# Kernel optimization log

Measured on AMD Instinct MI355X. Metric: run time of the kernel, lower is better.

The kernel has to match this reference:

```python
import jax, jax.numpy as jnp
import numpy as np

DIM = 512
HEADS = 8
DIM_HEAD = 64
B, N = 4, 2048
EPS = 1e-5


def setup_inputs() -> dict:
    key = jax.random.key(0)
    ks = jax.random.split(key, 6)
    s = 0.02
    x = jax.random.normal(ks[0], (B, N, DIM), dtype=jnp.float32)
    Wq = jax.random.normal(ks[1], (DIM, HEADS * DIM_HEAD), dtype=jnp.float32) * s
    Wkv = jax.random.normal(ks[2], (DIM, 2 * HEADS * DIM_HEAD), dtype=jnp.float32) * s
    Wo = jax.random.normal(ks[3], (HEADS * DIM_HEAD, DIM), dtype=jnp.float32) * s
    bo = jnp.zeros((DIM,), dtype=jnp.float32)
    # gating layer: torch init is weight=0, bias=1; randomize weight slightly for a nontrivial path
    Wg = jax.random.normal(ks[4], (DIM, HEADS * DIM_HEAD), dtype=jnp.float32) * s
    bg = jnp.ones((HEADS * DIM_HEAD,), dtype=jnp.float32)
    gamma = jnp.ones((DIM,), dtype=jnp.float32)
    beta = jnp.zeros((DIM,), dtype=jnp.float32)
    return {"x": x, "Wq": Wq, "Wkv": Wkv, "Wo": Wo, "bo": bo,
            "Wg": Wg, "bg": bg, "gamma": gamma, "beta": beta}


def reference(x, Wq, Wkv, Wo, bo, Wg, bg, gamma, beta):
    h, d = HEADS, DIM_HEAD
    scale = d ** -0.5
    b, n, _ = x.shape

    q = x @ Wq                                   # [b, n, h*d]
    kv = x @ Wkv                                 # [b, n, 2*h*d]
    k, v = jnp.split(kv, 2, axis=-1)

    def split_heads(t):
        return t.reshape(b, n, h, d).transpose(0, 2, 1, 3)  # [b, h, n, d]

    q = split_heads(q) * scale
    k = split_heads(k)
    v = split_heads(v)

    dots = jnp.einsum('bhid,bhjd->bhij', q, k)   # [b, h, n, n]
    attn = jax.nn.softmax(dots, axis=-1)
    out = jnp.einsum('bhij,bhjd->bhid', attn, v)  # [b, h, n, d]
    out = out.transpose(0, 2, 1, 3).reshape(b, n, h * d)

    gates = x @ Wg + bg                           # [b, n, h*d]
    out = out * jax.nn.sigmoid(gates)
    out = out @ Wo + bo                           # [b, n, dim]
    out = x + out

    # LayerNorm over last dim, eps=1e-5 (torch default)
    mu = jnp.mean(out, axis=-1, keepdims=True)
    var = jnp.var(out, axis=-1, keepdims=True)
    out = (out - mu) * jax.lax.rsqrt(var + EPS) * gamma + beta
    return out
```

## Files before the change

### kernel.cpp

```cpp
#include <hip/hip_runtime.h>
#include <hip/hip_bf16.h>
#include <stdint.h>
#include <stddef.h>

#define SEQ   2048
#define NBATCH 4
#define NHEAD  8
#define DMODEL 512

typedef __attribute__((ext_vector_type(8))) short bf16x8;
typedef __attribute__((ext_vector_type(4))) float f32x4;
typedef __attribute__((ext_vector_type(16))) float f32x16;

#define MFMA16(a, b, c) __builtin_amdgcn_mfma_f32_16x16x32_bf16(a, b, c, 0, 0, 0)
#define MFMA32(a, b, c) __builtin_amdgcn_mfma_f32_32x32x16_bf16(a, b, c, 0, 0, 0)

#define QSCALE 0.18033688011112042f

__device__ __forceinline__ float bf2f(ushort u) {
  union { uint32_t i; float f; } v; v.i = ((uint32_t)u) << 16; return v.f;
}
__device__ __forceinline__ ushort f2bf(float f) {
  union { float f; uint32_t i; } v; v.f = f;
  uint32_t u = v.i;
  return (ushort)((u + 0x7fffu + ((u >> 16) & 1u)) >> 16);
}
__device__ __forceinline__ uint32_t cvtpk(float lo, float hi) {
  uint32_t d;
  asm("v_cvt_pk_bf16_f32 %0, %1, %2" : "=v"(d) : "v"(lo), "v"(hi));
  return d;
}

#if __has_builtin(__builtin_amdgcn_global_load_lds)
__device__ __forceinline__ void gload16(const void* g, void* l) {
  __builtin_amdgcn_global_load_lds(
      (const __attribute__((address_space(1))) void*)g,
      (__attribute__((address_space(3))) void*)l, 16, 0, 0);
}
#define GLOAD_DIRECT 1
#else
#define GLOAD_DIRECT 0
#endif

__global__ __launch_bounds__(256) void prep_k(const float* __restrict__ x,
                                              const float* __restrict__ Wq,
                                              const float* __restrict__ Wkv,
                                              const float* __restrict__ Wg,
                                              const float* __restrict__ Wo,
                                              ushort* __restrict__ xb,
                                              ushort* __restrict__ WT,
                                              ushort* __restrict__ WoT) {
  __shared__ ushort tile[32][33];
  int t = threadIdx.x;
  if (blockIdx.x < 2048) {
    int i = blockIdx.x * 256 + t;
    const float4* p = (const float4*)(x + (size_t)i * 8);
    float4 a = p[0], b = p[1];
    union { int4 v; ushort u[8]; } o;
    o.u[0] = f2bf(a.x); o.u[1] = f2bf(a.y); o.u[2] = f2bf(a.z); o.u[3] = f2bf(a.w);
    o.u[4] = f2bf(b.x); o.u[5] = f2bf(b.y); o.u[6] = f2bf(b.z); o.u[7] = f2bf(b.w);
    *(int4*)(xb + (size_t)i * 8) = o.v;
    return;
  }
  int bidx = blockIdx.x - 2048;
  int bx = bidx % 80, by = bidx / 80;
  const float* W;
  ushort* dst;
  int N, nt;
  if (bx < 16)       { W = Wq;  dst = WT;              N = 512;  nt = bx; }
  else if (bx < 48)  { W = Wkv; dst = WT + 512 * 512;  N = 1024; nt = bx - 16; }
  else if (bx < 64)  { W = Wg;  dst = WT + 1536 * 512; N = 512;  nt = bx - 48; }
  else               { W = Wo;  dst = WoT;             N = 512;  nt = bx - 64; }
  int n0 = nt * 32, k0 = by * 32;
  int r = t >> 3, c = (t & 7) * 4;
#pragma unroll
  for (int j = 0; j < 4; j++)
    tile[r][c + j] = f2bf(W[(size_t)(k0 + r) * N + n0 + c + j]);
  __syncthreads();
#pragma unroll
  for (int j = 0; j < 4; j++)
    dst[(size_t)(n0 + r) * 512 + k0 + c + j] = tile[c + j][r];
}

__global__ __launch_bounds__(256, 2) void gemm128_k(const ushort* __restrict__ A,
                                                    const ushort* __restrict__ Bt,
                                                    ushort* __restrict__ qb,
                                                    ushort* __restrict__ kb,
                                                    ushort* __restrict__ vT,
                                                    ushort* __restrict__ gsb,
                                                    const float* __restrict__ bias) {
  __shared__ __align__(16) ushort Sh[4 * 128 * 64];
#define ASB(p) (Sh + (p) * (128 * 64))
#define BSB(p) (Sh + 2 * (128 * 64) + (p) * (128 * 64))
  int t = threadIdx.x;
  int nb = gridDim.x * gridDim.y;
  int bid = blockIdx.y * gridDim.x + blockIdx.x;
  int swz = (bid & 7) * (nb >> 3) + (bid >> 3);
  int row0 = (swz / gridDim.x) * 128, col0 = (swz % gridDim.x) * 128;

  int w = t >> 6, l = t & 63, l31 = l & 31, hi = l >> 5;
  int wm = w >> 1, wn = w & 1;
  f32x16 acc[2][2] = {};

  int srow = t >> 3;
  int ssl = (t & 7) ^ (srow & 7);
  const ushort* Ag = A + (size_t)(row0 + srow) * 512 + ssl * 8;
  const ushort* Bg = Bt + (size_t)(col0 + srow) * 512 + ssl * 8;
  int wslot = __builtin_amdgcn_readfirstlane((t >> 6) << 6);

#if GLOAD_DIRECT
#define STG(p, kt)                                                              \
  do {                                                                          \
    gload16(Ag + (size_t)(kt) * 64 + 0 * 32 * 512, ASB(p) + (wslot +   0) * 8); \
    gload16(Ag + (size_t)(kt) * 64 + 1 * 32 * 512, ASB(p) + (wslot + 256) * 8); \
    gload16(Ag + (size_t)(kt) * 64 + 2 * 32 * 512, ASB(p) + (wslot + 512) * 8); \
    gload16(Ag + (size_t)(kt) * 64 + 3 * 32 * 512, ASB(p) + (wslot + 768) * 8); \
    gload16(Bg + (size_t)(kt) * 64 + 0 * 32 * 512, BSB(p) + (wslot +   0) * 8); \
    gload16(Bg + (size_t)(kt) * 64 + 1 * 32 * 512, BSB(p) + (wslot + 256) * 8); \
    gload16(Bg + (size_t)(kt) * 64 + 2 * 32 * 512, BSB(p) + (wslot + 512) * 8); \
    gload16(Bg + (size_t)(kt) * 64 + 3 * 32 * 512, BSB(p) + (wslot + 768) * 8); \
  } while (0)
#else
#define STG(p, kt)                                                                  \
  do {                                                                              \
    *(int4*)(ASB(p) + (t +   0) * 8) = *(const int4*)(Ag + (size_t)(kt) * 64);      \
    *(int4*)(ASB(p) + (t + 256) * 8) =                                              \
        *(const int4*)(Ag + (size_t)(kt) * 64 + 1 * 32 * 512);                      \
    *(int4*)(ASB(p) + (t + 512) * 8) =                                              \
        *(const int4*)(Ag + (size_t)(kt) * 64 + 2 * 32 * 512);                      \
    *(int4*)(ASB(p) + (t + 768) * 8) =                                              \
        *(const int4*)(Ag + (size_t)(kt) * 64 + 3 * 32 * 512);                      \
    *(int4*)(BSB(p) + (t +   0) * 8) = *(const int4*)(Bg + (size_t)(kt) * 64);      \
    *(int4*)(BSB(p) + (t + 256) * 8) =                                              \
        *(const int4*)(Bg + (size_t)(kt) * 64 + 1 * 32 * 512);                      \
    *(int4*)(BSB(p) + (t + 512) * 8) =                                              \
        *(const int4*)(Bg + (size_t)(kt) * 64 + 2 * 32 * 512);                      \
    *(int4*)(BSB(p) + (t + 768) * 8) =                                              \
        *(const int4*)(Bg + (size_t)(kt) * 64 + 3 * 32 * 512);                      \
  } while (0)
#endif

#define FRAG(Mb, r, s) \
  (*(const bf16x8*)(Mb + ((r) * 64) + ((((s) ^ ((r) & 7))) << 3)))

  STG(0, 0);
  __syncthreads();

  for (int kt = 0; kt < 8; kt++) {
    int p = kt & 1;
    if (kt < 7) STG(p ^ 1, kt + 1);

    bf16x8 bfrag[2][4];
#pragma unroll
    for (int cb = 0; cb < 2; cb++)
#pragma unroll
      for (int kk = 0; kk < 4; kk++)
        bfrag[cb][kk] = FRAG(BSB(p), wn * 64 + cb * 32 + l31, kk * 2 + hi);

    __builtin_amdgcn_s_setprio(1);
#pragma unroll
    for (int rb = 0; rb < 2; rb++) {
      bf16x8 af[4];
#pragma unroll
      for (int kk = 0; kk < 4; kk++)
        af[kk] = FRAG(ASB(p), wm * 64 + rb * 32 + l31, kk * 2 + hi);
#pragma unroll
      for (int kk = 0; kk < 4; kk++) {
        acc[rb][0] = MFMA32(af[kk], bfrag[0][kk], acc[rb][0]);
        acc[rb][1] = MFMA32(af[kk], bfrag[1][kk], acc[rb][1]);
      }
    }
    __builtin_amdgcn_s_setprio(0);

    if (kt < 7) __syncthreads();
  }
#undef STG
#undef FRAG

  if (col0 >= 1024 && col0 < 1536) {
    __syncthreads();
    ushort* lt = Sh;
#pragma unroll
    for (int rb = 0; rb < 2; rb++)
#pragma unroll
      for (int cb = 0; cb < 2; cb++)
#pragma unroll
        for (int e = 0; e < 16; e++) {
          int rr = (e & 3) + 8 * (e >> 2) + 4 * hi;
          int rowL = wm * 64 + rb * 32 + rr;
          int colL = wn * 64 + cb * 32 + l31;
          lt[colL * 136 + rowL] = f2bf(acc[rb][cb][e]);
        }
    __syncthreads();
    int b_ = row0 >> 11;
    int nb0 = row0 & 2047;
#pragma unroll
    for (int r = 0; r < 8; r++) {
      int lin = r * 256 + t;
      int dcol = lin >> 4, n8 = lin & 15;
      int vcol = (col0 - 1024) + dcol;
      int hh = vcol >> 6, dd = vcol & 63;
      bf16x8 v = *(const bf16x8*)(lt + dcol * 136 + n8 * 8);
      *(bf16x8*)(vT + (((size_t)(b_ * 8 + hh) * 64) + dd) * 2048 + nb0 + n8 * 8) = v;
    }
  } else {
#pragma unroll
    for (int rb = 0; rb < 2; rb++) {
#pragma unroll
      for (int cb = 0; cb < 2; cb++) {
#pragma unroll
        for (int e = 0; e < 16; e++) {
          int rr = (e & 3) + 8 * (e >> 2) + 4 * hi;
          int row = row0 + wm * 64 + rb * 32 + rr;
          int col = col0 + wn * 64 + cb * 32 + l31;
          float v = acc[rb][cb][e];
          if (col0 < 512) {
            qb[(size_t)row * 512 + col] = f2bf(v * QSCALE);
          } else if (col0 < 1024) {
            kb[(size_t)row * 512 + (col - 512)] = f2bf(v);
          } else {
            v += bias[col - 1536];
            v = 1.f / (1.f + __expf(-v));
            gsb[(size_t)row * 512 + (col - 1536)] = f2bf(v);
          }
        }
      }
    }
  }
#undef ASB
#undef BSB
}

__global__ __launch_bounds__(256, 2) void gemm_o_k(const ushort* __restrict__ A,
                                                   const ushort* __restrict__ Bt,
                                                   float* __restrict__ yout,
                                                   const float* __restrict__ bias,
                                                   const float* __restrict__ res) {
  __shared__ __align__(16) ushort As[2][128 * 64];
  __shared__ __align__(16) ushort Bs[2][64 * 64];
  int t = threadIdx.x;
  int nb = gridDim.x * gridDim.y;
  int bid = blockIdx.y * gridDim.x + blockIdx.x;
  int swz = (bid & 7) * (nb >> 3) + (bid >> 3);
  int row0 = (swz / gridDim.x) * 128, col0 = (swz % gridDim.x) * 64;

  int w = t >> 6, l = t & 63, l31 = l & 31, hi = l >> 5;
  int wm = w >> 1, wn = w & 1;
  f32x16 acc[2] = {};

  int srow = t >> 3;
  int ssl = (t & 7) ^ (srow & 7);
  const ushort* Ag = A + (size_t)(row0 + srow) * 512 + ssl * 8;
  const ushort* Bg = Bt + (size_t)(col0 + srow) * 512 + ssl * 8;
  int wslot = __builtin_amdgcn_readfirstlane((t >> 6) << 6);

#if GLOAD_DIRECT
#define STG(p, kt)                                                                \
  do {                                                                            \
    gload16(Ag + (size_t)(kt) * 64 + 0 * 32 * 512, &As[p][(wslot +   0) * 8]);    \
    gload16(Ag + (size_t)(kt) * 64 + 1 * 32 * 512, &As[p][(wslot + 256) * 8]);    \
    gload16(Ag + (size_t)(kt) * 64 + 2 * 32 * 512, &As[p][(wslot + 512) * 8]);    \
    gload16(Ag + (size_t)(kt) * 64 + 3 * 32 * 512, &As[p][(wslot + 768) * 8]);    \
    gload16(Bg + (size_t)(kt) * 64 + 0 * 32 * 512, &Bs[p][(wslot +   0) * 8]);    \
    gload16(Bg + (size_t)(kt) * 64 + 1 * 32 * 512, &Bs[p][(wslot + 256) * 8]);    \
  } while (0)
#else
#define STG(p, kt)                                                                  \
  do {                                                                              \
    *(int4*)(&As[p][(t +   0) * 8]) = *(const int4*)(Ag + (size_t)(kt) * 64);       \
    *(int4*)(&As[p][(t + 256) * 8]) =                                               \
        *(const int4*)(Ag + (size_t)(kt) * 64 + 1 * 32 * 512);                      \
    *(int4*)(&As[p][(t + 512) * 8]) =                                               \
        *(const int4*)(Ag + (size_t)(kt) * 64 + 2 * 32 * 512);                      \
    *(int4*)(&As[p][(t + 768) * 8]) =                                               \
        *(const int4*)(Ag + (size_t)(kt) * 64 + 3 * 32 * 512);                      \
    *(int4*)(&Bs[p][(t +   0) * 8]) = *(const int4*)(Bg + (size_t)(kt) * 64);       \
    *(int4*)(&Bs[p][(t + 256) * 8]) =                                               \
        *(const int4*)(Bg + (size_t)(kt) * 64 + 1 * 32 * 512);                      \
  } while (0)
#endif

#define FRAG(Mb, r, s) \
  (*(const bf16x8*)(&(Mb)[((r) * 64) + ((((s) ^ ((r) & 7))) << 3)]))

  STG(0, 0);
  __syncthreads();

  for (int kt = 0; kt < 8; kt++) {
    int p = kt & 1;
    if (kt < 7) STG(p ^ 1, kt + 1);

    bf16x8 bfrag[4];
#pragma unroll
    for (int kk = 0; kk < 4; kk++)
      bfrag[kk] = FRAG(Bs[p], wn * 32 + l31, kk * 2 + hi);

    __builtin_amdgcn_s_setprio(1);
#pragma unroll
    for (int rb = 0; rb < 2; rb++) {
      bf16x8 af[4];
#pragma unroll
      for (int kk = 0; kk < 4; kk++)
        af[kk] = FRAG(As[p], wm * 64 + rb * 32 + l31, kk * 2 + hi);
#pragma unroll
      for (int kk = 0; kk < 4; kk++)
        acc[rb] = MFMA32(af[kk], bfrag[kk], acc[rb]);
    }
    __builtin_amdgcn_s_setprio(0);

    if (kt < 7) __syncthreads();
  }
#undef STG
#undef FRAG

#pragma unroll
  for (int rb = 0; rb < 2; rb++) {
#pragma unroll
    for (int e = 0; e < 16; e++) {
      int rr = (e & 3) + 8 * (e >> 2) + 4 * hi;
      int row = row0 + wm * 64 + rb * 32 + rr;
      int col = col0 + wn * 32 + l31;
      float v = acc[rb][e] + bias[col] + res[(size_t)row * 512 + col];
      yout[(size_t)row * 512 + col] = v;
    }
  }
}

__global__ __launch_bounds__(512) void attn_k(const ushort* __restrict__ q,
                                              const ushort* __restrict__ kbuf,
                                              const ushort* __restrict__ vT,
                                              const ushort* __restrict__ gs,
                                              ushort* __restrict__ gated) {
  __shared__ __align__(16) ushort Kl[2][2][64][72];
  __shared__ __align__(16) ushort Vl[2][2][64][72];
  int t = threadIdx.x;
  int bid = blockIdx.x;
  int swz = (bid & 7) * 32 + (bid >> 3);
  int qt = swz & 7, bh = swz >> 3;
  int b = bh >> 3, h = bh & 7;
  int q0 = qt * 256;
  int w = t >> 6, l = t & 63;
  int l31 = l & 31, hi = l >> 5;
  size_t base_n = (size_t)b * SEQ;

  const ushort* qp = q + (base_n + q0 + w * 32 + l31) * 512 + h * 64 + hi * 8;
  bf16x8 qf[4];
#pragma unroll
  for (int kd = 0; kd < 4; kd++)
    qf[kd] = *(const bf16x8*)(qp + kd * 16);

  bf16x8 vones;
#pragma unroll
  for (int j = 0; j < 8; j++) vones[j] = (short)0x3F80;

  f32x16 acco0 = {}, acco1 = {}, acco2 = {};

  int srow = t >> 3, c8 = (t & 7) * 8;
  const ushort* kg = kbuf + (base_n + srow) * 512 + h * 64 + c8;
  const ushort* vg = vT + ((size_t)bh * 64 + srow) * 2048 + c8;

#define QK_PHASE(KB, S0, S1)                                                   \
  do {                                                                         \
    _Pragma("unroll")                                                          \
    for (int kd = 0; kd < 4; kd++) {                                           \
      bf16x8 k0 = *(const bf16x8*)((KB) + l31 * 144 + kd * 32 + hi * 16);      \
      bf16x8 k1 = *(const bf16x8*)((KB) + (32 + l31) * 144 + kd * 32 + hi * 16);\
      S0 = MFMA32(k0, qf[kd], S0);                                             \
      S1 = MFMA32(k1, qf[kd], S1);                                             \
    }                                                                          \
  } while (0)

#define SM_PHASE(S0, S1, PK)                                                   \
  do {                                                                         \
    _Pragma("unroll")                                                          \
    for (int sg = 0; sg < 4; sg++) {                                           \
      _Pragma("unroll")                                                        \
      for (int u = 0; u < 2; u++) {                                            \
        float a = __builtin_amdgcn_exp2f(S0[(sg << 2) | (u << 1)]);            \
        float c = __builtin_amdgcn_exp2f(S0[(sg << 2) | (u << 1) | 1]);        \
        PK[sg * 2 + u] = cvtpk(a, c);                                          \
      }                                                                        \
    }                                                                          \
    _Pragma("unroll")                                                          \
    for (int sg = 0; sg < 4; sg++) {                                           \
      _Pragma("unroll")                                                        \
      for (int u = 0; u < 2; u++) {                                            \
        float a = __builtin_amdgcn_exp2f(S1[(sg << 2) | (u << 1)]);            \
        float c = __builtin_amdgcn_exp2f(S1[(sg << 2) | (u << 1) | 1]);        \
        PK[8 + sg * 2 + u] = cvtpk(a, c);                                      \
      }                                                                        \
    }                                                                          \
  } while (0)

#define PV_PHASE(VB, PK)                                                       \
  do {                                                                         \
    _Pragma("unroll")                                                          \
    for (int jk = 0; jk < 4; jk++) {                                           \
      uint32_t x0 = PK[(2 * jk) * 2 + 0], y0 = PK[(2 * jk + 1) * 2 + 0];       \
      uint32_t x1 = PK[(2 * jk) * 2 + 1], y1 = PK[(2 * jk + 1) * 2 + 1];       \
      asm("v_permlane32_swap_b32 %0, %1" : "+v"(x0), "+v"(y0));                \
      asm("v_permlane32_swap_b32 %0, %1" : "+v"(x1), "+v"(y1));                \
      union { bf16x8 v; uint32_t u[4]; } pa;                                   \
      pa.u[0] = x0; pa.u[1] = x1; pa.u[2] = y0; pa.u[3] = y1;                  \
      bf16x8 v0 = *(const bf16x8*)((VB) + l31 * 144 + jk * 32 + hi * 16);      \
      bf16x8 v1 = *(const bf16x8*)((VB) + (32 + l31) * 144 + jk * 32 + hi * 16);\
      acco0 = MFMA32(pa.v, v0, acco0);                                         \
      acco1 = MFMA32(pa.v, v1, acco1);                                         \
      acco2 = MFMA32(pa.v, vones, acco2);                                      \
    }                                                                          \
  } while (0)

#define STAGE_LDS(pp)                                                          \
  do {                                                                         \
    *(int4*)((char*)Kl[pp][0] + srow * 144 + c8 * 2) = kA;                     \
    *(int4*)((char*)Kl[pp][1] + srow * 144 + c8 * 2) = kB;                     \
    *(int4*)((char*)Vl[pp][0] + srow * 144 + c8 * 2) = vA;                     \
    *(int4*)((char*)Vl[pp][1] + srow * 144 + c8 * 2) = vB;                     \
  } while (0)

#define LOADT(n)                                                               \
  do {                                                                         \
    kA = *(const int4*)(kg + (size_t)(n) * 128 * 512);                         \
    kB = *(const int4*)(kg + ((size_t)(n) * 128 + 64) * 512);                  \
    vA = *(const int4*)(vg + (n) * 128);                                       \
    vB = *(const int4*)(vg + (n) * 128 + 64);                                  \
  } while (0)

  int4 kA, kB, vA, vB;
  LOADT(0);
  STAGE_LDS(0);
  LOADT(1);
  __syncthreads();

  int p = 0;
  const int NT = SEQ / 128;
  for (int jt = 0; jt < NT; jt++) {
    f32x16 s0 = {}, s1 = {};
    __builtin_amdgcn_s_setprio(1);
    QK_PHASE((const char*)Kl[p][0], s0, s1);
    __builtin_amdgcn_s_setprio(0);
    if (jt < NT - 1) STAGE_LDS(p ^ 1);
    {
      uint32_t pk[16];
      SM_PHASE(s0, s1, pk);
      __builtin_amdgcn_s_setprio(1);
      PV_PHASE((const char*)Vl[p][0], pk);
      __builtin_amdgcn_s_setprio(0);
    }
    s0 = (f32x16){}; s1 = (f32x16){};
    __builtin_amdgcn_s_setprio(1);
    QK_PHASE((const char*)Kl[p][1], s0, s1);
    __builtin_amdgcn_s_setprio(0);
    {
      uint32_t pk[16];
      SM_PHASE(s0, s1, pk);
      __builtin_amdgcn_s_setprio(1);
      PV_PHASE((const char*)Vl[p][1], pk);
      __builtin_amdgcn_s_setprio(0);
    }

    if (jt < NT - 1) {
      __syncthreads();
      if (jt < NT - 2) LOADT(jt + 2);
      p ^= 1;
    }
  }
#undef QK_PHASE
#undef SM_PHASE
#undef PV_PHASE
#undef STAGE_LDS
#undef LOADT

#pragma unroll
  for (int e = 0; e < 16; e++) {
    int qr = (e & 3) + 8 * (e >> 2) + 4 * hi;
    size_t row = base_n + q0 + w * 32 + qr;
    int col = h * 64 + l31;
    float rcp = 1.f / acco2[e];
    float v0 = acco0[e] * rcp * bf2f(gs[row * 512 + col]);
    float v1 = acco1[e] * rcp * bf2f(gs[row * 512 + col + 32]);
    gated[row * 512 + col] = f2bf(v0);
    gated[row * 512 + col + 32] = f2bf(v1);
  }
}

__global__ __launch_bounds__(256) void ln_k(const float* __restrict__ y,
                                            const float* __restrict__ gamma,
                                            const float* __restrict__ beta,
                                            float* __restrict__ out) {
  int w = threadIdx.x >> 6, l = threadIdx.x & 63;
  size_t row = (size_t)blockIdx.x * 4 + w;
  const float4* yp = (const float4*)(y + row * 512);
  float4 a = yp[l * 2], b = yp[l * 2 + 1];
  float f[8] = {a.x, a.y, a.z, a.w, b.x, b.y, b.z, b.w};
  float sm = 0.f, sq = 0.f;
#pragma unroll
  for (int j = 0; j < 8; j++) { sm += f[j]; sq += f[j] * f[j]; }
#pragma unroll
  for (int off = 1; off < 64; off <<= 1) {
    sm += __shfl_xor(sm, off);
    sq += __shfl_xor(sq, off);
  }
  float mean = sm * (1.f / 512.f);
  float var = sq * (1.f / 512.f) - mean * mean;
  float rs = rsqrtf(var + 1e-5f);
  float4 g0 = ((const float4*)gamma)[l * 2], g1 = ((const float4*)gamma)[l * 2 + 1];
  float4 b0 = ((const float4*)beta)[l * 2],  b1 = ((const float4*)beta)[l * 2 + 1];
  float4 o0, o1;
  o0.x = (f[0] - mean) * rs * g0.x + b0.x;
  o0.y = (f[1] - mean) * rs * g0.y + b0.y;
  o0.z = (f[2] - mean) * rs * g0.z + b0.z;
  o0.w = (f[3] - mean) * rs * g0.w + b0.w;
  o1.x = (f[4] - mean) * rs * g1.x + b1.x;
  o1.y = (f[5] - mean) * rs * g1.y + b1.y;
  o1.z = (f[6] - mean) * rs * g1.z + b1.z;
  o1.w = (f[7] - mean) * rs * g1.w + b1.w;
  float4* op = (float4*)(out + row * 512);
  op[l * 2] = o0;
  op[l * 2 + 1] = o1;
}

extern "C" void kernel_launch(void* const* d_in, const int* in_sizes, int n_in,
                              void* d_out, int out_size, void* d_ws, size_t ws_size,
                              hipStream_t stream) {
  (void)in_sizes; (void)n_in; (void)out_size; (void)ws_size;
  const float* x     = (const float*)d_in[0];
  const float* Wq    = (const float*)d_in[1];
  const float* Wkv   = (const float*)d_in[2];
  const float* Wo    = (const float*)d_in[3];
  const float* bo    = (const float*)d_in[4];
  const float* Wg    = (const float*)d_in[5];
  const float* bg    = (const float*)d_in[6];
  const float* gamma = (const float*)d_in[7];
  const float* beta  = (const float*)d_in[8];

  char* ws = (char*)d_ws;
  ushort* xb    = (ushort*)(ws);
  ushort* qbuf  = (ushort*)(ws + (8u  << 20));
  ushort* kbuf  = (ushort*)(ws + (16u << 20));
  ushort* vT    = (ushort*)(ws + (32u << 20));
  ushort* gsb   = (ushort*)(ws + (40u << 20));
  ushort* gated = (ushort*)(ws + (48u << 20));
  float*  y     = (float*)(ws + (56u << 20));
  ushort* WT    = (ushort*)(ws + (72u << 20));
  ushort* WoT   = (ushort*)(ws + (74u << 20));

  prep_k<<<2048 + 1280, 256, 0, stream>>>(x, Wq, Wkv, Wg, Wo, xb, WT, WoT);

  gemm128_k<<<dim3(16, 64), 256, 0, stream>>>(xb, WT, qbuf, kbuf, vT, gsb, bg);

  attn_k<<<256, 512, 0, stream>>>(qbuf, kbuf, vT, gsb, gated);

  gemm_o_k<<<dim3(8, 64), 256, 0, stream>>>(gated, WoT, y, bo, x);

  ln_k<<<(NBATCH * SEQ) / 4, 256, 0, stream>>>(y, gamma, beta, (float*)d_out);
}
```

Baseline: 110.6 us.

## Pre-pack QKV/gate weights in MFMA fragment order and load B from global

```diff
diff --git a/kernel.cpp b/kernel.cpp
--- a/kernel.cpp
+++ b/kernel.cpp
@@ -65,33 +65,43 @@
   int bidx = blockIdx.x - 2048;
   int bx = bidx % 80, by = bidx / 80;
   const float* W;
-  ushort* dst;
-  int N, nt;
-  if (bx < 16)       { W = Wq;  dst = WT;              N = 512;  nt = bx; }
-  else if (bx < 48)  { W = Wkv; dst = WT + 512 * 512;  N = 1024; nt = bx - 16; }
-  else if (bx < 64)  { W = Wg;  dst = WT + 1536 * 512; N = 512;  nt = bx - 48; }
-  else               { W = Wo;  dst = WoT;             N = 512;  nt = bx - 64; }
+  int N, nt, base_n;
+  bool frag = true;
+  if (bx < 16)       { W = Wq;  N = 512;  nt = bx;      base_n = 0; }
+  else if (bx < 48)  { W = Wkv; N = 1024; nt = bx - 16; base_n = 512; }
+  else if (bx < 64)  { W = Wg;  N = 512;  nt = bx - 48; base_n = 1536; }
+  else               { W = Wo;  N = 512;  nt = bx - 64; base_n = 0; frag = false; }
   int n0 = nt * 32, k0 = by * 32;
   int r = t >> 3, c = (t & 7) * 4;
 #pragma unroll
   for (int j = 0; j < 4; j++)
     tile[r][c + j] = f2bf(W[(size_t)(k0 + r) * N + n0 + c + j]);
   __syncthreads();
-#pragma unroll
-  for (int j = 0; j < 4; j++)
-    dst[(size_t)(n0 + r) * 512 + k0 + c + j] = tile[c + j][r];
+  if (frag) {
+    int n = base_n + n0 + r;
+    int kbase = k0 + c;
+    int c5 = n >> 5, l31 = n & 31;
+    int ks = kbase >> 4, hi = (kbase >> 3) & 1;
+    size_t chunk = (size_t)(c5 * 32 + ks) * 64 + l31 + hi * 32;
+#pragma unroll
+    for (int j = 0; j < 4; j++)
+      WT[chunk * 8 + (kbase & 7) + j] = tile[c + j][r];
+  } else {
+#pragma unroll
+    for (int j = 0; j < 4; j++)
+      WoT[(size_t)(n0 + r) * 512 + k0 + c + j] = tile[c + j][r];
+  }
 }
 
 __global__ __launch_bounds__(256, 2) void gemm128_k(const ushort* __restrict__ A,
-                                                    const ushort* __restrict__ Bt,
+                                                    const ushort* __restrict__ Bf,
                                                     ushort* __restrict__ qb,
                                                     ushort* __restrict__ kb,
                                                     ushort* __restrict__ vT,
                                                     ushort* __restrict__ gsb,
                                                     const float* __restrict__ bias) {
-  __shared__ __align__(16) ushort Sh[4 * 128 * 64];
+  __shared__ __align__(16) ushort Sh[17408];
 #define ASB(p) (Sh + (p) * (128 * 64))
-#define BSB(p) (Sh + 2 * (128 * 64) + (p) * (128 * 64))
   int t = threadIdx.x;
   int nb = gridDim.x * gridDim.y;
   int bid = blockIdx.y * gridDim.x + blockIdx.x;
@@ -105,8 +115,10 @@
   int srow = t >> 3;
   int ssl = (t & 7) ^ (srow & 7);
   const ushort* Ag = A + (size_t)(row0 + srow) * 512 + ssl * 8;
-  const ushort* Bg = Bt + (size_t)(col0 + srow) * 512 + ssl * 8;
   int wslot = __builtin_amdgcn_readfirstlane((t >> 6) << 6);
+
+  const ushort* Bf0 = Bf + ((size_t)((col0 >> 5) + wn * 2 + 0) * 2048 + l) * 8;
+  const ushort* Bf1 = Bf + ((size_t)((col0 >> 5) + wn * 2 + 1) * 2048 + l) * 8;
 
 #if GLOAD_DIRECT
 #define STG(p, kt)                                                              \
@@ -115,10 +127,6 @@
     gload16(Ag + (size_t)(kt) * 64 + 1 * 32 * 512, ASB(p) + (wslot + 256) * 8); \
     gload16(Ag + (size_t)(kt) * 64 + 2 * 32 * 512, ASB(p) + (wslot + 512) * 8); \
     gload16(Ag + (size_t)(kt) * 64 + 3 * 32 * 512, ASB(p) + (wslot + 768) * 8); \
-    gload16(Bg + (size_t)(kt) * 64 + 0 * 32 * 512, BSB(p) + (wslot +   0) * 8); \
-    gload16(Bg + (size_t)(kt) * 64 + 1 * 32 * 512, BSB(p) + (wslot + 256) * 8); \
-    gload16(Bg + (size_t)(kt) * 64 + 2 * 32 * 512, BSB(p) + (wslot + 512) * 8); \
-    gload16(Bg + (size_t)(kt) * 64 + 3 * 32 * 512, BSB(p) + (wslot + 768) * 8); \
   } while (0)
 #else
 #define STG(p, kt)                                                                  \
@@ -130,13 +138,6 @@
         *(const int4*)(Ag + (size_t)(kt) * 64 + 2 * 32 * 512);                      \
     *(int4*)(ASB(p) + (t + 768) * 8) =                                              \
         *(const int4*)(Ag + (size_t)(kt) * 64 + 3 * 32 * 512);                      \
-    *(int4*)(BSB(p) + (t +   0) * 8) = *(const int4*)(Bg + (size_t)(kt) * 64);      \
-    *(int4*)(BSB(p) + (t + 256) * 8) =                                              \
-        *(const int4*)(Bg + (size_t)(kt) * 64 + 1 * 32 * 512);                      \
-    *(int4*)(BSB(p) + (t + 512) * 8) =                                              \
-        *(const int4*)(Bg + (size_t)(kt) * 64 + 2 * 32 * 512);                      \
-    *(int4*)(BSB(p) + (t + 768) * 8) =                                              \
-        *(const int4*)(Bg + (size_t)(kt) * 64 + 3 * 32 * 512);                      \
   } while (0)
 #endif
 
@@ -146,16 +147,17 @@
   STG(0, 0);
   __syncthreads();
 
+#pragma unroll
   for (int kt = 0; kt < 8; kt++) {
     int p = kt & 1;
     if (kt < 7) STG(p ^ 1, kt + 1);
 
     bf16x8 bfrag[2][4];
 #pragma unroll
-    for (int cb = 0; cb < 2; cb++)
-#pragma unroll
-      for (int kk = 0; kk < 4; kk++)
-        bfrag[cb][kk] = FRAG(BSB(p), wn * 64 + cb * 32 + l31, kk * 2 + hi);
+    for (int kk = 0; kk < 4; kk++) {
+      bfrag[0][kk] = *(const bf16x8*)(Bf0 + (kt * 4 + kk) * 512);
+      bfrag[1][kk] = *(const bf16x8*)(Bf1 + (kt * 4 + kk) * 512);
+    }
 
     __builtin_amdgcn_s_setprio(1);
 #pragma unroll
@@ -228,7 +230,6 @@
     }
   }
 #undef ASB
-#undef BSB
 }
 
 __global__ __launch_bounds__(256, 2) void gemm_o_k(const ushort* __restrict__ A,
```

New measurement: 111.2 us. About the same (+0.5%).

## Rewrite QKVG projection GEMM with 256x128 tiles and triple-buffered staging

Applied to the files above, without the earlier changes.

```diff
diff --git a/kernel.cpp b/kernel.cpp
--- a/kernel.cpp
+++ b/kernel.cpp
@@ -82,21 +82,20 @@
     dst[(size_t)(n0 + r) * 512 + k0 + c + j] = tile[c + j][r];
 }
 
-__global__ __launch_bounds__(256, 2) void gemm128_k(const ushort* __restrict__ A,
-                                                    const ushort* __restrict__ Bt,
-                                                    ushort* __restrict__ qb,
-                                                    ushort* __restrict__ kb,
-                                                    ushort* __restrict__ vT,
-                                                    ushort* __restrict__ gsb,
-                                                    const float* __restrict__ bias) {
-  __shared__ __align__(16) ushort Sh[4 * 128 * 64];
-#define ASB(p) (Sh + (p) * (128 * 64))
-#define BSB(p) (Sh + 2 * (128 * 64) + (p) * (128 * 64))
+__global__ __launch_bounds__(512) void gemm_qkvg_p(const ushort* __restrict__ A,
+                                                   const ushort* __restrict__ Bt,
+                                                   ushort* __restrict__ qb,
+                                                   ushort* __restrict__ kb,
+                                                   ushort* __restrict__ vT,
+                                                   ushort* __restrict__ gsb,
+                                                   const float* __restrict__ bias) {
+  __shared__ __align__(16) ushort Sh[3 * 24576];
+#define AB(b) (Sh + (b) * 24576)
+#define BB(b) (Sh + (b) * 24576 + 16384)
   int t = threadIdx.x;
-  int nb = gridDim.x * gridDim.y;
   int bid = blockIdx.y * gridDim.x + blockIdx.x;
-  int swz = (bid & 7) * (nb >> 3) + (bid >> 3);
-  int row0 = (swz / gridDim.x) * 128, col0 = (swz % gridDim.x) * 128;
+  int swz = (bid & 7) * 64 + (bid >> 3);
+  int row0 = (swz >> 4) * 256, col0 = (swz & 15) * 128;
 
   int w = t >> 6, l = t & 63, l31 = l & 31, hi = l >> 5;
   int wm = w >> 1, wn = w & 1;
@@ -109,72 +108,72 @@
   int wslot = __builtin_amdgcn_readfirstlane((t >> 6) << 6);
 
 #if GLOAD_DIRECT
-#define STG(p, kt)                                                              \
-  do {                                                                          \
-    gload16(Ag + (size_t)(kt) * 64 + 0 * 32 * 512, ASB(p) + (wslot +   0) * 8); \
-    gload16(Ag + (size_t)(kt) * 64 + 1 * 32 * 512, ASB(p) + (wslot + 256) * 8); \
-    gload16(Ag + (size_t)(kt) * 64 + 2 * 32 * 512, ASB(p) + (wslot + 512) * 8); \
-    gload16(Ag + (size_t)(kt) * 64 + 3 * 32 * 512, ASB(p) + (wslot + 768) * 8); \
-    gload16(Bg + (size_t)(kt) * 64 + 0 * 32 * 512, BSB(p) + (wslot +   0) * 8); \
-    gload16(Bg + (size_t)(kt) * 64 + 1 * 32 * 512, BSB(p) + (wslot + 256) * 8); \
-    gload16(Bg + (size_t)(kt) * 64 + 2 * 32 * 512, BSB(p) + (wslot + 512) * 8); \
-    gload16(Bg + (size_t)(kt) * 64 + 3 * 32 * 512, BSB(p) + (wslot + 768) * 8); \
-  } while (0)
+#define STGA(b, kt, j)                                                   \
+  gload16(Ag + (size_t)(kt) * 64 + (size_t)(j) * 64 * 512,               \
+          AB(b) + ((size_t)wslot + (j) * 512) * 8)
+#define STGB(b, kt, j)                                                   \
+  gload16(Bg + (size_t)(kt) * 64 + (size_t)(j) * 64 * 512,               \
+          BB(b) + ((size_t)wslot + (j) * 512) * 8)
 #else
-#define STG(p, kt)                                                                  \
-  do {                                                                              \
-    *(int4*)(ASB(p) + (t +   0) * 8) = *(const int4*)(Ag + (size_t)(kt) * 64);      \
-    *(int4*)(ASB(p) + (t + 256) * 8) =                                              \
-        *(const int4*)(Ag + (size_t)(kt) * 64 + 1 * 32 * 512);                      \
-    *(int4*)(ASB(p) + (t + 512) * 8) =                                              \
-        *(const int4*)(Ag + (size_t)(kt) * 64 + 2 * 32 * 512);                      \
-    *(int4*)(ASB(p) + (t + 768) * 8) =                                              \
-        *(const int4*)(Ag + (size_t)(kt) * 64 + 3 * 32 * 512);                      \
-    *(int4*)(BSB(p) + (t +   0) * 8) = *(const int4*)(Bg + (size_t)(kt) * 64);      \
-    *(int4*)(BSB(p) + (t + 256) * 8) =                                              \
-        *(const int4*)(Bg + (size_t)(kt) * 64 + 1 * 32 * 512);                      \
-    *(int4*)(BSB(p) + (t + 512) * 8) =                                              \
-        *(const int4*)(Bg + (size_t)(kt) * 64 + 2 * 32 * 512);                      \
-    *(int4*)(BSB(p) + (t + 768) * 8) =                                              \
-        *(const int4*)(Bg + (size_t)(kt) * 64 + 3 * 32 * 512);                      \
-  } while (0)
+#define STGA(b, kt, j)                                                   \
+  (*(int4*)(AB(b) + ((size_t)t + (j) * 512) * 8) =                       \
+       *(const int4*)(Ag + (size_t)(kt) * 64 + (size_t)(j) * 64 * 512))
+#define STGB(b, kt, j)                                                   \
+  (*(int4*)(BB(b) + ((size_t)t + (j) * 512) * 8) =                       \
+       *(const int4*)(Bg + (size_t)(kt) * 64 + (size_t)(j) * 64 * 512))
 #endif
 
 #define FRAG(Mb, r, s) \
   (*(const bf16x8*)(Mb + ((r) * 64) + ((((s) ^ ((r) & 7))) << 3)))
 
-  STG(0, 0);
-  __syncthreads();
-
-  for (int kt = 0; kt < 8; kt++) {
-    int p = kt & 1;
-    if (kt < 7) STG(p ^ 1, kt + 1);
-
-    bf16x8 bfrag[2][4];
-#pragma unroll
-    for (int cb = 0; cb < 2; cb++)
-#pragma unroll
-      for (int kk = 0; kk < 4; kk++)
-        bfrag[cb][kk] = FRAG(BSB(p), wn * 64 + cb * 32 + l31, kk * 2 + hi);
-
-    __builtin_amdgcn_s_setprio(1);
-#pragma unroll
-    for (int rb = 0; rb < 2; rb++) {
-      bf16x8 af[4];
-#pragma unroll
-      for (int kk = 0; kk < 4; kk++)
-        af[kk] = FRAG(ASB(p), wm * 64 + rb * 32 + l31, kk * 2 + hi);
-#pragma unroll
-      for (int kk = 0; kk < 4; kk++) {
-        acc[rb][0] = MFMA32(af[kk], bfrag[0][kk], acc[rb][0]);
-        acc[rb][1] = MFMA32(af[kk], bfrag[1][kk], acc[rb][1]);
+  STGA(0, 0, 0); STGA(0, 0, 1); STGA(0, 0, 2); STGA(0, 0, 3);
+  STGB(0, 0, 0); STGB(0, 0, 1);
+  STGA(1, 1, 0); STGA(1, 1, 1); STGA(1, 1, 2); STGA(1, 1, 3);
+  STGB(1, 1, 0); STGB(1, 1, 1);
+  __builtin_amdgcn_sched_barrier(0);
+  asm volatile("s_waitcnt vmcnt(6)" ::: "memory");
+  __builtin_amdgcn_s_barrier();
+  __builtin_amdgcn_sched_barrier(0);
+
+  for (int k = 0; k < 8; k++) {
+    int bk = k % 3, bp = (k + 2) % 3;
+    const ushort* Abuf = AB(bk);
+    const ushort* Bbuf = BB(bk);
+    bool pf = (k + 2) < 8;
+#pragma unroll
+    for (int q = 0; q < 4; q++) {
+      bf16x8 af0 = FRAG(Abuf, wm * 64 + 0 * 32 + l31, q * 2 + hi);
+      bf16x8 af1 = FRAG(Abuf, wm * 64 + 1 * 32 + l31, q * 2 + hi);
+      bf16x8 bf0 = FRAG(Bbuf, wn * 64 + 0 * 32 + l31, q * 2 + hi);
+      bf16x8 bf1 = FRAG(Bbuf, wn * 64 + 1 * 32 + l31, q * 2 + hi);
+      if (pf) {
+        if (q == 0)      { STGA(bp, k + 2, 0); STGA(bp, k + 2, 1); }
+        else if (q == 1) { STGA(bp, k + 2, 2); STGA(bp, k + 2, 3); }
+        else if (q == 2) { STGB(bp, k + 2, 0); STGB(bp, k + 2, 1); }
       }
-    }
-    __builtin_amdgcn_s_setprio(0);
-
-    if (kt < 7) __syncthreads();
-  }
-#undef STG
+      __builtin_amdgcn_sched_barrier(0);
+      __builtin_amdgcn_s_barrier();
+      asm volatile("s_waitcnt lgkmcnt(0)" ::: "memory");
+      __builtin_amdgcn_sched_barrier(0);
+      __builtin_amdgcn_s_setprio(1);
+      acc[0][0] = MFMA32(af0, bf0, acc[0][0]);
+      acc[0][1] = MFMA32(af0, bf1, acc[0][1]);
+      acc[1][0] = MFMA32(af1, bf0, acc[1][0]);
+      acc[1][1] = MFMA32(af1, bf1, acc[1][1]);
+      __builtin_amdgcn_s_setprio(0);
+      if (q < 3) {
+        __builtin_amdgcn_s_barrier();
+      } else if (k < 7) {
+        __builtin_amdgcn_sched_barrier(0);
+        if (k < 6) asm volatile("s_waitcnt vmcnt(6)" ::: "memory");
+        else       asm volatile("s_waitcnt vmcnt(0)" ::: "memory");
+        __builtin_amdgcn_s_barrier();
+        __builtin_amdgcn_sched_barrier(0);
+      }
+    }
+  }
+#undef STGA
+#undef STGB
 #undef FRAG
 
   if (col0 >= 1024 && col0 < 1536) {
@@ -189,18 +188,18 @@
           int rr = (e & 3) + 8 * (e >> 2) + 4 * hi;
           int rowL = wm * 64 + rb * 32 + rr;
           int colL = wn * 64 + cb * 32 + l31;
-          lt[colL * 136 + rowL] = f2bf(acc[rb][cb][e]);
+          lt[colL * 264 + rowL] = f2bf(acc[rb][cb][e]);
         }
     __syncthreads();
     int b_ = row0 >> 11;
     int nb0 = row0 & 2047;
 #pragma unroll
     for (int r = 0; r < 8; r++) {
-      int lin = r * 256 + t;
-      int dcol = lin >> 4, n8 = lin & 15;
+      int lin = r * 512 + t;
+      int dcol = lin >> 5, n8 = lin & 31;
       int vcol = (col0 - 1024) + dcol;
       int hh = vcol >> 6, dd = vcol & 63;
-      bf16x8 v = *(const bf16x8*)(lt + dcol * 136 + n8 * 8);
+      bf16x8 v = *(const bf16x8*)(lt + dcol * 264 + n8 * 8);
       *(bf16x8*)(vT + (((size_t)(b_ * 8 + hh) * 64) + dd) * 2048 + nb0 + n8 * 8) = v;
     }
   } else {
@@ -227,8 +226,8 @@
       }
     }
   }
-#undef ASB
-#undef BSB
+#undef AB
+#undef BB
 }
 
 __global__ __launch_bounds__(256, 2) void gemm_o_k(const ushort* __restrict__ A,
@@ -547,7 +546,7 @@
 
   prep_k<<<2048 + 1280, 256, 0, stream>>>(x, Wq, Wkv, Wg, Wo, xb, WT, WoT);
 
-  gemm128_k<<<dim3(16, 64), 256, 0, stream>>>(xb, WT, qbuf, kbuf, vT, gsb, bg);
+  gemm_qkvg_p<<<dim3(16, 32), 512, 0, stream>>>(xb, WT, qbuf, kbuf, vT, gsb, bg);
 
   attn_k<<<256, 512, 0, stream>>>(qbuf, kbuf, vT, gsb, gated);
 
```

New measurement: 114.0 us. 3.0% more time.
